# Performance work log

Hardware: AMD Instinct MI355X
Metric: run time of the kernel (lower is better)

Reference implementation:

```python
import jax, jax.numpy as jnp
import numpy as np


def _segment_mean(msg, dst, num_nodes):
    # msg: [E, B, O, T] summed into [N, B, O, T], mean over incoming edges
    s = jax.ops.segment_sum(msg, dst, num_segments=num_nodes)
    cnt = jax.ops.segment_sum(jnp.ones((msg.shape[0],), msg.dtype), dst, num_segments=num_nodes)
    return s / jnp.clip(cnt, 1.0)[:, None, None, None]


def _gcn(x, edge_index, edge_attr, A, Wk, Wr, b):
    # Edge-conditioned (spline-style) graph conv.
    # x: [B, N, Cin, T]; edge_attr: [E, 3]; Wk: [K, Cin, Cout]
    N = x.shape[1]
    src, dst = edge_index[0], edge_index[1]
    Bw = jax.nn.softmax(edge_attr @ A, axis=-1)          # [E, K] basis weights
    We = jnp.einsum('ek,kio->eio', Bw, Wk)                # [E, Cin, Cout]
    msg = jnp.einsum('beit,eio->ebot', x[:, src], We)     # [E, B, Cout, T]
    agg = _segment_mean(msg, dst, N).transpose(1, 0, 2, 3)  # [B, N, Cout, T]
    out = agg + jnp.einsum('bnit,io->bnot', x, Wr) + b[None, None, :, None]
    return jax.nn.elu(out)


def _pool(x, P, C, T):
    # x: [B, N_l, C, T] -> flatten, sparse-pool with P [N_{l+1}, N_l], unflatten
    B, N = x.shape[0], x.shape[1]
    xf = x.reshape(B, N, C * T)
    xf = jnp.einsum('mn,bnf->bmf', P, xf)
    return xf.reshape(B, P.shape[0], C, T)


def setup_inputs() -> dict:
    key = jax.random.key(0)
    ks = jax.random.split(key, 24)
    B, T = 2, 200
    N = [2048, 512, 128, 64]
    E = [16384, 8192, 2048]
    nf = [1, 8, 16, 32, 64, 128, 128]
    ld = 64

    def rn(k, shape, scale=1.0):
        return jax.random.normal(k, shape, dtype=jnp.float32) * scale

    inp = {}
    inp['x'] = rn(ks[0], (B, N[0], nf[0], T))
    inp['ei0'] = jax.random.randint(ks[1], (2, E[0]), 0, N[0])
    inp['ea0'] = jax.random.uniform(ks[2], (E[0], 3), dtype=jnp.float32)
    inp['ei1'] = jax.random.randint(ks[3], (2, E[1]), 0, N[1])
    inp['ea1'] = jax.random.uniform(ks[4], (E[1], 3), dtype=jnp.float32)
    inp['ei2'] = jax.random.randint(ks[5], (2, E[2]), 0, N[2])
    inp['ea2'] = jax.random.uniform(ks[6], (E[2], 3), dtype=jnp.float32)
    # gcn params: (A basis map, K=3 kernel weights, root weight, bias)
    inp['A1'] = rn(ks[7], (3, 3))
    inp['Wk1'] = rn(ks[8], (3, nf[0], nf[2]), 1.0 / np.sqrt(nf[0]))
    inp['Wr1'] = rn(ks[9], (nf[0], nf[2]), 1.0 / np.sqrt(nf[0]))
    inp['b1'] = jnp.zeros((nf[2],), jnp.float32)
    inp['A2'] = rn(ks[10], (3, 3))
    inp['Wk2'] = rn(ks[11], (3, nf[2], nf[3]), 1.0 / np.sqrt(nf[2]))
    inp['Wr2'] = rn(ks[12], (nf[2], nf[3]), 1.0 / np.sqrt(nf[2]))
    inp['b2'] = jnp.zeros((nf[3],), jnp.float32)
    inp['A3'] = rn(ks[13], (3, 3))
    inp['Wk3'] = rn(ks[14], (3, nf[3], nf[4]), 1.0 / np.sqrt(nf[3]))
    inp['Wr3'] = rn(ks[15], (nf[3], nf[4]), 1.0 / np.sqrt(nf[3]))
    inp['b3'] = jnp.zeros((nf[4],), jnp.float32)
    # sparse pooling projections (dense here)
    inp['P01'] = rn(ks[16], (N[1], N[0]), 1.0 / np.sqrt(N[0]))
    inp['P12'] = rn(ks[17], (N[2], N[1]), 1.0 / np.sqrt(N[1]))
    inp['P23'] = rn(ks[18], (N[3], N[2]), 1.0 / np.sqrt(N[2]))
    # 1x1 conv encoder head
    inp['fce1_w'] = rn(ks[19], (nf[4], nf[6]), 1.0 / np.sqrt(nf[4]))
    inp['fce1_b'] = jnp.zeros((nf[6],), jnp.float32)
    inp['fce2_w'] = rn(ks[20], (nf[6], ld), 1.0 / np.sqrt(nf[6]))
    inp['fce2_b'] = jnp.zeros((ld,), jnp.float32)
    return inp


def reference(x, ei0, ea0, ei1, ea1, ei2, ea2, A1, Wk1, Wr1, b1, A2, Wk2, Wr2, b2,
              A3, Wk3, Wr3, b3, P01, P12, P23, fce1_w, fce1_b, fce2_w, fce2_b):
    T = x.shape[-1]
    # level 0 -> 1
    h = _gcn(x, ei0, ea0, A1, Wk1, Wr1, b1)          # [B, N0, 16, T]
    h = _pool(h, P01, h.shape[2], T)                 # [B, N1, 16, T]
    # level 1 -> 2
    h = _gcn(h, ei1, ea1, A2, Wk2, Wr2, b2)          # [B, N1, 32, T]
    h = _pool(h, P12, h.shape[2], T)                 # [B, N2, 32, T]
    # level 2 -> 3
    h = _gcn(h, ei2, ea2, A3, Wk3, Wr3, b3)          # [B, N2, 64, T]
    h = _pool(h, P23, h.shape[2], T)                 # [B, N3, 64, T]
    # 1x1 conv encoder head (channel-wise linear over node/time grid)
    h = jax.nn.elu(jnp.einsum('bnct,co->bnot', h, fce1_w) + fce1_b[None, None, :, None])
    mu = jnp.tanh(jnp.einsum('bnct,co->bnot', h, fce2_w) + fce2_b[None, None, :, None])
    return mu  # [B, N3, latent_dim, T]
```

## Files before the change

### kernel.cpp

```cpp
#include <hip/hip_runtime.h>
#include <hip/hip_bf16.h>

using bf16 = __hip_bfloat16;
typedef unsigned short ushort_t;
typedef unsigned int uint_t;

constexpr int B = 2, T = 200;
constexpr int N0 = 2048, N1 = 512, N2 = 128, N3 = 64;
constexpr int E0 = 16384, E1 = 8192, E2 = 2048;

typedef __attribute__((ext_vector_type(8))) short bf16x8;
typedef __attribute__((ext_vector_type(4))) float f32x4;

constexpr size_t O_FLAG = 161792;
constexpr size_t O_WC1  = 163840;
constexpr size_t O_BIAS = 164096;
constexpr size_t O_BW0  = 165312;
constexpr size_t O_BW1  = 361920;
constexpr size_t O_BW2  = 460224;
constexpr size_t O_PB1  = 484800;
constexpr size_t O_PB2  = 2581952;
constexpr size_t O_PB3  = 2713024;
constexpr size_t O_WT2  = 2729408;
constexpr size_t O_WT3  = 2733504;
constexpr size_t O_W1H  = 2749888;
constexpr size_t O_W2H  = 2766272;
constexpr size_t O_AA   = 2785280;
constexpr size_t O_BB   = 15892480;

__device__ __forceinline__ float ldx(const void* p, long i, int bf) {
  if (bf) {
    uint_t v = (uint_t)(((const ushort_t*)p)[i]) << 16;
    float f; __builtin_memcpy(&f, &v, 4); return f;
  }
  return ((const float*)p)[i];
}
__device__ __forceinline__ ushort_t f2bfu(float v) {
  bf16 h = __float2bfloat16(v); ushort_t u; __builtin_memcpy(&u, &h, 2); return u;
}

struct InPtrs {
  const void* ea0; const void* ea1; const void* ea2;
  const void* P01; const void* P12; const void* P23;
  const void* Wk1; const void* Wr1; const void* Wk2; const void* Wr2;
  const void* Wk3; const void* Wr3; const void* W1h; const void* W2h;
  const void* b1; const void* b2; const void* b3; const void* b1h; const void* b2h;
  const void* A1; const void* A2; const void* A3;
};

__global__ void k_setup0(int* I, const ushort_t* ea) {
  if (blockIdx.x < 158) {
    int i = blockIdx.x * 256 + threadIdx.x;
    I[i] = 0;
  } else if (threadIdx.x == 0) {
    int c = 0;
    for (int i = 0; i < 128; ++i) {
      uint_t v = (uint_t)ea[i] << 16;
      float f; __builtin_memcpy(&f, &v, 4);
      if (f >= 0.f && f <= 1.0f) c++;
    }
    *(int*)((char*)I + O_FLAG) = (c >= 120) ? 1 : 0;
  }
}

__device__ __forceinline__ void bw_one(const void* ea, int bf, const void* A,
                                       float* bw, int e) {
  float a0 = ldx(ea, e*3+0, bf), a1 = ldx(ea, e*3+1, bf), a2 = ldx(ea, e*3+2, bf);
  float l0 = a0*ldx(A,0,bf) + a1*ldx(A,3,bf) + a2*ldx(A,6,bf);
  float l1 = a0*ldx(A,1,bf) + a1*ldx(A,4,bf) + a2*ldx(A,7,bf);
  float l2 = a0*ldx(A,2,bf) + a1*ldx(A,5,bf) + a2*ldx(A,8,bf);
  float m = fmaxf(l0, fmaxf(l1, l2));
  float x0 = expf(l0 - m), x1 = expf(l1 - m), x2 = expf(l2 - m);
  float inv = 1.0f / (x0 + x1 + x2);
  bw[e*3+0] = x0*inv; bw[e*3+1] = x1*inv; bw[e*3+2] = x2*inv;
}

__global__ void k_prep(InPtrs P, char* base) {
  int bf = *(const int*)(base + O_FLAG);
  int bx = blockIdx.x, tid = threadIdx.x;
  float* bw0 = (float*)(base + O_BW0);
  float* bw1 = (float*)(base + O_BW1);
  float* bw2 = (float*)(base + O_BW2);
  if (bx < 64)        { bw_one(P.ea0, bf, P.A1, bw0, bx*256+tid); return; }
  if (bx < 96)        { bw_one(P.ea1, bf, P.A2, bw1, (bx-64)*256+tid); return; }
  if (bx < 104)       { bw_one(P.ea2, bf, P.A3, bw2, (bx-96)*256+tid); return; }
  if (bx < 4200)      { long i = (long)(bx-104)*256+tid;
                        ((ushort_t*)(base+O_PB1))[i] = f2bfu(ldx(P.P01, i, bf)); return; }
  if (bx < 4456)      { int i = (bx-4200)*256+tid;
                        ((ushort_t*)(base+O_PB2))[i] = f2bfu(ldx(P.P12, i, bf)); return; }
  if (bx < 4488)      { int i = (bx-4456)*256+tid;
                        ((ushort_t*)(base+O_PB3))[i] = f2bfu(ldx(P.P23, i, bf)); return; }
  if (bx < 4496)      { int j = (bx-4488)*256+tid; int o = j>>6, c = j&63;
                        float v = (c<48) ? ldx(P.Wk2, c*32+o, bf) : ldx(P.Wr2, (c-48)*32+o, bf);
                        ((ushort_t*)(base+O_WT2))[j] = f2bfu(v); return; }
  if (bx < 4528)      { int j = (bx-4496)*256+tid; int o = j>>7, c = j&127;
                        float v = (c<96) ? ldx(P.Wk3, c*64+o, bf) : ldx(P.Wr3, (c-96)*64+o, bf);
                        ((ushort_t*)(base+O_WT3))[j] = f2bfu(v); return; }
  if (bx < 4560)      { int j = (bx-4528)*256+tid; int o = j>>6, c = j&63;
                        ((ushort_t*)(base+O_W1H))[j] = f2bfu(ldx(P.W1h, c*128+o, bf)); return; }
  if (bx < 4592)      { int j = (bx-4560)*256+tid; int o = j>>7, c = j&127;
                        ((ushort_t*)(base+O_W2H))[j] = f2bfu(ldx(P.W2h, c*64+o, bf)); return; }
  {
    int i = (bx-4592)*256+tid;
    if (i < 64) {
      ((float*)(base+O_WC1))[i] = (i<48) ? ldx(P.Wk1, i, bf) : ldx(P.Wr1, i-48, bf);
    } else if (i < 368) {
      int j = i - 64; float v;
      if (j < 16)       v = ldx(P.b1, j, bf);
      else if (j < 48)  v = ldx(P.b2, j-16, bf);
      else if (j < 112) v = ldx(P.b3, j-48, bf);
      else if (j < 240) v = ldx(P.b1h, j-112, bf);
      else              v = ldx(P.b2h, j-240, bf);
      ((float*)(base+O_BIAS))[j] = v;
    }
  }
}

__global__ void k_hist3(const int* d0, const int* d1, const int* d2,
                        int* c0, int* c1, int* c2) {
  int i = blockIdx.x * 256 + threadIdx.x;
  if (i < E0) atomicAdd(&c0[d0[i]], 1);
  if (i < E1) atomicAdd(&c1[d1[i]], 1);
  if (i < E2) atomicAdd(&c2[d2[i]], 1);
}

__global__ void k_scan3(const int* c0, int* o0, int* u0,
                        const int* c1, int* o1, int* u1,
                        const int* c2, int* o2, int* u2) {
  const int* cnt; int* off; int* cur; int N;
  if (blockIdx.x == 0)      { cnt = c0; off = o0; cur = u0; N = N0; }
  else if (blockIdx.x == 1) { cnt = c1; off = o1; cur = u1; N = N1; }
  else                      { cnt = c2; off = o2; cur = u2; N = N2; }
  int tid = threadIdx.x;
  int chunk = (N + 63) >> 6;
  int base = tid * chunk;
  int s = 0;
  for (int j = 0; j < chunk; ++j) { int idx = base + j; if (idx < N) s += cnt[idx]; }
  int pre = s;
  for (int d = 1; d < 64; d <<= 1) {
    int v = __shfl_up(pre, d, 64);
    if (tid >= d) pre += v;
  }
  int run = pre - s;
  for (int j = 0; j < chunk; ++j) {
    int idx = base + j;
    if (idx < N) { off[idx] = run; cur[idx] = run; run += cnt[idx]; }
  }
  if (tid == 63) off[N] = run;
}

__global__ void k_fill3(const int* d0, int* u0, int* e0l,
                        const int* d1, int* u1, int* e1l,
                        const int* d2, int* u2, int* e2l) {
  int i = blockIdx.x * 256 + threadIdx.x;
  if (i < E0) { int p = atomicAdd(&u0[d0[i]], 1); e0l[p] = i; }
  if (i < E1) { int p = atomicAdd(&u1[d1[i]], 1); e1l[p] = i; }
  if (i < E2) { int p = atomicAdd(&u2[d2[i]], 1); e2l[p] = i; }
}

__global__ __launch_bounds__(256) void k_gc1(const void* x, const int* src,
    const int* off, const int* elist, const int* cnt, const float* bw,
    const float* W, const float* bias, bf16* h1, const int* flagp) {
  __shared__ float Wl[64];
  __shared__ float bl[16];
  __shared__ float ew0[32], ew1[32], ew2[32];
  __shared__ int es[32];
  int tid = threadIdx.x;
  if (tid < 64) Wl[tid] = W[tid];
  if (tid < 16) bl[tid] = bias[tid];
  int bf = *flagp;
  int n = blockIdx.y, b = blockIdx.z;
  int t = tid;
  bool tok = t < T;
  int beg = off[n], end = off[n + 1];
  float a0 = 0.f, a1 = 0.f, a2 = 0.f;
  for (int q0 = beg; q0 < end; q0 += 32) {
    int m = end - q0; if (m > 32) m = 32;
    __syncthreads();
    if (tid < m) {
      int e = elist[q0 + tid];
      es[tid] = src[e];
      ew0[tid] = bw[e*3+0]; ew1[tid] = bw[e*3+1]; ew2[tid] = bw[e*3+2];
    }
    __syncthreads();
    if (tok) {
      for (int j = 0; j < m; ++j) {
        float xv = ldx(x, (long)(b * N0 + es[j]) * T + t, bf);
        a0 += ew0[j] * xv; a1 += ew1[j] * xv; a2 += ew2[j] * xv;
      }
    }
  }
  __syncthreads();
  if (!tok) return;
  int c = cnt[n];
  float inv = 1.f / (float)(c > 0 ? c : 1);
  a0 *= inv; a1 *= inv; a2 *= inv;
  float xr = ldx(x, (long)(b * N0 + n) * T + t, bf);
  bf16* op = h1 + ((long)(b * N0 + n) * 16) * T + t;
#pragma unroll
  for (int o = 0; o < 16; ++o) {
    float v = a0 * Wl[o] + a1 * Wl[16 + o] + a2 * Wl[32 + o] + xr * Wl[48 + o] + bl[o];
    v = v > 0.f ? v : (expf(v) - 1.f);
    op[o * T] = __float2bfloat16(v);
  }
}

template<int CIN, int CPI, int O>
__global__ __launch_bounds__(256) void k_gcm(const float* hp, const int* src,
    const int* off, const int* elist, const int* cnt, const float* bw,
    const ushort_t* Wt, const float* bias, bf16* h, int N) {
  constexpr int C = 4 * CIN;
  constexpr int KG = C / 8;
  constexpr int MT = O / 16;
  __shared__ __align__(16) ushort_t Ws[O * C];
  __shared__ __align__(16) ushort_t Is[64 * C];
  __shared__ float ew0[32], ew1[32], ew2[32];
  __shared__ int es[32];
  int tid = threadIdx.x;
  int w = tid >> 6, l = tid & 63;
  int lf = l & 15, quad = l >> 4;
  int t0 = blockIdx.x * 64;
  int n = blockIdx.y, b = blockIdx.z;
  {
    const uint4* Wg = (const uint4*)Wt;
    for (int s = tid; s < O * KG; s += 256) {
      int o = s / KG, kg = s % KG;
      *(uint4*)(Ws + o * C + ((kg ^ (o & 7)) * 8)) = Wg[s];
    }
  }
  int tx = tid & 63, iy = tid >> 6;
  int t = t0 + tx;
  bool tok = t < T;
  float acc[3][CPI], xr[CPI];
#pragma unroll
  for (int k = 0; k < 3; ++k)
#pragma unroll
    for (int j = 0; j < CPI; ++j) acc[k][j] = 0.f;
#pragma unroll
  for (int j = 0; j < CPI; ++j) xr[j] = 0.f;
  int beg = off[n], end = off[n + 1];
  for (int q0 = beg; q0 < end; q0 += 32) {
    int mE = end - q0; if (mE > 32) mE = 32;
    __syncthreads();
    if (tid < mE) {
      int e = elist[q0 + tid];
      es[tid] = src[e];
      ew0[tid] = bw[e*3+0]; ew1[tid] = bw[e*3+1]; ew2[tid] = bw[e*3+2];
    }
    __syncthreads();
    if (tok) {
      for (int j2 = 0; j2 < mE; ++j2) {
        int s = es[j2];
        float w0 = ew0[j2], w1 = ew1[j2], w2 = ew2[j2];
        const float* xp = hp + ((long)(b * N + s) * CIN) * T + t;
#pragma unroll
        for (int j = 0; j < CPI; ++j) {
          float xv = xp[(iy * CPI + j) * T];
          acc[0][j] += w0 * xv; acc[1][j] += w1 * xv; acc[2][j] += w2 * xv;
        }
      }
    }
  }
  float inv = 1.f;
  if (tok) {
    int c = cnt[n];
    inv = 1.f / (float)(c > 0 ? c : 1);
    const float* xs = hp + ((long)(b * N + n) * CIN) * T + t;
#pragma unroll
    for (int j = 0; j < CPI; ++j) xr[j] = xs[(iy * CPI + j) * T];
  }
#pragma unroll
  for (int j = 0; j < CPI; ++j) {
    int i = iy * CPI + j;
#pragma unroll
    for (int k = 0; k < 3; ++k) {
      int c = k * CIN + i;
      Is[tx * C + ((c >> 3) ^ (tx & 7)) * 8 + (c & 7)] = f2bfu(acc[k][j] * inv);
    }
    int c = 3 * CIN + i;
    Is[tx * C + ((c >> 3) ^ (tx & 7)) * 8 + (c & 7)] = f2bfu(xr[j]);
  }
  __syncthreads();
  f32x4 dacc[MT];
#pragma unroll
  for (int mt = 0; mt < MT; ++mt) dacc[mt] = (f32x4){0.f, 0.f, 0.f, 0.f};
  int tr = w * 16 + lf;
#pragma unroll
  for (int kc = 0; kc < C / 32; ++kc) {
    int kg0 = kc * 4 + quad;
    bf16x8 bfr = *(const bf16x8*)(Is + tr * C + ((kg0 ^ (tr & 7)) * 8));
#pragma unroll
    for (int mt = 0; mt < MT; ++mt) {
      int o = mt * 16 + lf;
      bf16x8 afr = *(const bf16x8*)(Ws + o * C + ((kg0 ^ (o & 7)) * 8));
      dacc[mt] = __builtin_amdgcn_mfma_f32_16x16x32_bf16(afr, bfr, dacc[mt], 0, 0, 0);
    }
  }
  int tg = t0 + w * 16 + lf;
  if (tg < T) {
    long nb = (long)(b * N + n) * O;
#pragma unroll
    for (int mt = 0; mt < MT; ++mt) {
#pragma unroll
      for (int r = 0; r < 4; ++r) {
        int o = mt * 16 + quad * 4 + r;
        float v = dacc[mt][r] + bias[o];
        v = v > 0.f ? v : (expf(v) - 1.f);
        h[(nb + o) * T + tg] = __float2bfloat16(v);
      }
    }
  }
}

template<int FT>
__global__ __launch_bounds__(256) void k_poolw(const ushort_t* __restrict__ Pb,
    const ushort_t* __restrict__ h, float* __restrict__ out,
    int M, int K, int F, int nInner) {
  constexpr int BN = 16 * FT;
  constexpr int NOCT = BN / 8;
  constexpr int NROW = 256 / NOCT;
  constexpr int NP = 64 / NROW;
  __shared__ __align__(16) ushort_t As[64 * 64];
  __shared__ __align__(16) ushort_t Bs[BN * 64];
  int tid = threadIdx.x;
  int w = tid >> 6, l = tid & 63;
  int lf = l & 15, quad = l >> 4;
  int ml = w * 16 + lf;
  int v = blockIdx.x;
  { int q = gridDim.x >> 3; v = (v & 7) * q + (v >> 3); }
  int f_blk = v / nInner; int rem = v - f_blk * nInner;
  int m_blk = rem >> 1;
  int b = rem & 1;
  int f0 = f_blk * BN, m0 = m_blk * 64;

  int am0 = tid >> 3, ak = tid & 7;
  int am1 = am0 + 32;
  const ushort_t* Ap0 = Pb + (long)(m0 + am0) * K + ak * 8;
  const ushort_t* Ap1 = Pb + (long)(m0 + am1) * K + ak * 8;
  int wofA0 = am0 * 64 + ((ak ^ (am0 & 7)) * 8);
  int wofA1 = am1 * 64 + ((ak ^ (am1 & 7)) * 8);
  int fo = tid % NOCT;
  int krb = tid / NOCT;
  const ushort_t* Bp = h + ((long)b * K + krb) * F + f0 + fo * 8;

  f32x4 acc[FT];
#pragma unroll
  for (int ft = 0; ft < FT; ++ft) acc[ft] = (f32x4){0.f, 0.f, 0.f, 0.f};

  for (int kk = 0; kk < K; kk += 64) {
    uint4 a0 = *(const uint4*)(Ap0 + kk);
    uint4 a1 = *(const uint4*)(Ap1 + kk);
    uint4 bv[NP];
#pragma unroll
    for (int p = 0; p < NP; ++p)
      bv[p] = *(const uint4*)(Bp + (long)(kk + p * NROW) * F);
    __syncthreads();
    *(uint4*)(As + wofA0) = a0;
    *(uint4*)(As + wofA1) = a1;
#pragma unroll
    for (int p = 0; p < NP; ++p) {
      int kr = krb + p * NROW;
      int kh = kr >> 3, kw = kr & 7;
#pragma unroll
      for (int j = 0; j < 8; ++j) {
        int f = fo * 8 + j;
        int sw = j ^ fo;
        Bs[f * 64 + ((kh ^ sw) * 8) + kw] = ((const ushort_t*)&bv[p])[j];
      }
    }
    __syncthreads();
#pragma unroll
    for (int ks = 0; ks < 2; ++ks) {
      int kq = ks * 4 + quad;
      bf16x8 bfr[FT];
#pragma unroll
      for (int ft = 0; ft < FT; ++ft) {
        int fl = ft * 16 + lf;
        int sfl = (fl & 7) ^ ((fl >> 3) & 7);
        bfr[ft] = *(const bf16x8*)(Bs + fl * 64 + ((kq ^ sfl) * 8));
      }
      bf16x8 afr = *(const bf16x8*)(As + ml * 64 + ((kq ^ (ml & 7)) * 8));
#pragma unroll
      for (int ft = 0; ft < FT; ++ft)
        acc[ft] = __builtin_amdgcn_mfma_f32_16x16x32_bf16(afr, bfr[ft], acc[ft], 0, 0, 0);
    }
  }

#pragma unroll
  for (int rr = 0; rr < 4; ++rr) {
    int m = m0 + w * 16 + quad * 4 + rr;
    float* op = out + ((long)(b * M + m)) * F + f0 + lf;
#pragma unroll
    for (int ft = 0; ft < FT; ++ft) op[ft * 16] = acc[ft][rr];
  }
}

__global__ __launch_bounds__(256) void k_head(const float* hp3, const ushort_t* W1t,
    const ushort_t* W2t, const float* bias, void* outp, const int* flagp) {
  __shared__ __align__(16) ushort_t Ws1[128 * 64];
  __shared__ __align__(16) ushort_t Ws2[64 * 128];
  __shared__ __align__(16) ushort_t Is[64 * 64];
  __shared__ __align__(16) ushort_t G[64 * 128];
  int tid = threadIdx.x;
  int w = tid >> 6, l = tid & 63;
  int lf = l & 15, quad = l >> 4;
  int t0 = blockIdx.x * 64;
  int n = blockIdx.y, b = blockIdx.z;
  {
    const uint4* g1 = (const uint4*)W1t;
    for (int s = tid; s < 1024; s += 256) {
      int o = s >> 3, kg = s & 7;
      *(uint4*)(Ws1 + o * 64 + ((kg ^ (o & 7)) * 8)) = g1[s];
    }
    const uint4* g2 = (const uint4*)W2t;
    for (int s = tid; s < 1024; s += 256) {
      int o = s >> 4, kg = s & 15;
      *(uint4*)(Ws2 + o * 128 + ((kg ^ (o & 7)) * 8)) = g2[s];
    }
  }
  {
    int t = tid & 63;
    bool tok = (t0 + t) < T;
    const float* ip = hp3 + ((long)(b * 64 + n) * 64) * T + t0;
    for (int kg = tid >> 6; kg < 8; kg += 4) {
      ushort_t r[8];
#pragma unroll
      for (int j = 0; j < 8; ++j)
        r[j] = tok ? f2bfu(ip[(kg * 8 + j) * T + t]) : (ushort_t)0;
      *(uint4*)(Is + t * 64 + ((kg ^ (t & 7)) * 8)) = *(uint4*)r;
    }
  }
  __syncthreads();
  int tr = w * 16 + lf;
  {
    f32x4 a1[8];
#pragma unroll
    for (int mt = 0; mt < 8; ++mt) a1[mt] = (f32x4){0.f, 0.f, 0.f, 0.f};
#pragma unroll
    for (int kc = 0; kc < 2; ++kc) {
      int kg0 = kc * 4 + quad;
      bf16x8 bfr = *(const bf16x8*)(Is + tr * 64 + ((kg0 ^ (tr & 7)) * 8));
#pragma unroll
      for (int mt = 0; mt < 8; ++mt) {
        int o = mt * 16 + lf;
        bf16x8 afr = *(const bf16x8*)(Ws1 + o * 64 + ((kg0 ^ (o & 7)) * 8));
        a1[mt] = __builtin_amdgcn_mfma_f32_16x16x32_bf16(afr, bfr, a1[mt], 0, 0, 0);
      }
    }
    int tG = w * 16 + lf;
#pragma unroll
    for (int mt = 0; mt < 8; ++mt) {
#pragma unroll
      for (int r = 0; r < 4; ++r) {
        int o1 = mt * 16 + quad * 4 + r;
        float v = a1[mt][r] + bias[112 + o1];
        v = v > 0.f ? v : (expf(v) - 1.f);
        G[tG * 128 + ((o1 >> 3) ^ (tG & 7)) * 8 + (o1 & 7)] = f2bfu(v);
      }
    }
  }
  __syncthreads();
  {
    f32x4 a2[4];
#pragma unroll
    for (int mt = 0; mt < 4; ++mt) a2[mt] = (f32x4){0.f, 0.f, 0.f, 0.f};
#pragma unroll
    for (int kc = 0; kc < 4; ++kc) {
      int kg0 = kc * 4 + quad;
      bf16x8 bfr = *(const bf16x8*)(G + tr * 128 + ((kg0 ^ (tr & 7)) * 8));
#pragma unroll
      for (int mt = 0; mt < 4; ++mt) {
        int o = mt * 16 + lf;
        bf16x8 afr = *(const bf16x8*)(Ws2 + o * 128 + ((kg0 ^ (o & 7)) * 8));
        a2[mt] = __builtin_amdgcn_mfma_f32_16x16x32_bf16(afr, bfr, a2[mt], 0, 0, 0);
      }
    }
    int t = t0 + w * 16 + lf;
    if (t < T) {
      int bf = *flagp;
      long nb = (long)(b * 64 + n) * 64;
#pragma unroll
      for (int mt = 0; mt < 4; ++mt) {
#pragma unroll
        for (int r = 0; r < 4; ++r) {
          int o2 = mt * 16 + quad * 4 + r;
          float v = tanhf(a2[mt][r] + bias[240 + o2]);
          long idx = (nb + o2) * T + t;
          if (bf) ((bf16*)outp)[idx] = __float2bfloat16(v);
          else    ((float*)outp)[idx] = v;
        }
      }
    }
  }
}

extern "C" void kernel_launch(void* const* d_in, const int* in_sizes, int n_in,
                              void* d_out, int out_size, void* d_ws, size_t ws_size,
                              hipStream_t stream) {
  const int* ei0 = (const int*)d_in[1];
  const int* ei1 = (const int*)d_in[3];
  const int* ei2 = (const int*)d_in[5];

  char* base = (char*)d_ws;
  int* I = (int*)base;
  int* cnt0 = I;         int* off0 = I + 2048;  int* cur0 = I + 4112;  int* el0 = I + 6160;
  int* cnt1 = I + 22544; int* off1 = I + 23056; int* cur1 = I + 23584; int* el1 = I + 24096;
  int* cnt2 = I + 32288; int* off2 = I + 32416; int* cur2 = I + 32560; int* el2 = I + 32688;
  const int* flagp = (const int*)(base + O_FLAG);
  float* wc1f = (float*)(base + O_WC1);
  float* bias = (float*)(base + O_BIAS);
  float* bw0 = (float*)(base + O_BW0);
  float* bw1 = (float*)(base + O_BW1);
  float* bw2 = (float*)(base + O_BW2);
  ushort_t* Pb1 = (ushort_t*)(base + O_PB1);
  ushort_t* Pb2 = (ushort_t*)(base + O_PB2);
  ushort_t* Pb3 = (ushort_t*)(base + O_PB3);
  ushort_t* wt2 = (ushort_t*)(base + O_WT2);
  ushort_t* wt3 = (ushort_t*)(base + O_WT3);
  ushort_t* w1t = (ushort_t*)(base + O_W1H);
  ushort_t* w2t = (ushort_t*)(base + O_W2H);
  char* Aa = base + O_AA;
  char* Bb = base + O_BB;

  InPtrs P = { d_in[2], d_in[4], d_in[6], d_in[19], d_in[20], d_in[21],
               d_in[8], d_in[9], d_in[12], d_in[13], d_in[16], d_in[17],
               d_in[22], d_in[24], d_in[10], d_in[14], d_in[18], d_in[23],
               d_in[25], d_in[7], d_in[11], d_in[15] };

  k_setup0<<<159, 256, 0, stream>>>(I, (const ushort_t*)d_in[2]);
  k_prep<<<4594, 256, 0, stream>>>(P, base);
  k_hist3<<<64, 256, 0, stream>>>(ei0 + E0, ei1 + E1, ei2 + E2, cnt0, cnt1, cnt2);
  k_scan3<<<3, 64, 0, stream>>>(cnt0, off0, cur0, cnt1, off1, cur1, cnt2, off2, cur2);
  k_fill3<<<64, 256, 0, stream>>>(ei0 + E0, cur0, el0, ei1 + E1, cur1, el1, ei2 + E2, cur2, el2);

  k_gc1<<<dim3(1, N0, B), 256, 0, stream>>>(d_in[0], ei0, off0, el0, cnt0, bw0, wc1f, bias, (bf16*)Bb, flagp);
  k_poolw<2><<<1600, 256, 0, stream>>>(Pb1, (const ushort_t*)Bb, (float*)Aa, 512, 2048, 3200, 16);
  k_gcm<16, 4, 32><<<dim3(4, N1, B), 256, 0, stream>>>((const float*)Aa, ei1, off1, el1, cnt1, bw1, wt2, bias + 16, (bf16*)Bb, N1);
  k_poolw<2><<<800, 256, 0, stream>>>(Pb2, (const ushort_t*)Bb, (float*)Aa, 128, 512, 6400, 4);
  k_gcm<32, 8, 64><<<dim3(4, N2, B), 256, 0, stream>>>((const float*)Aa, ei2, off2, el2, cnt2, bw2, wt3, bias + 48, (bf16*)Bb, N2);
  k_poolw<2><<<800, 256, 0, stream>>>(Pb3, (const ushort_t*)Bb, (float*)Aa, 64, 128, 12800, 2);
  k_head<<<dim3(4, N3, B), 256, 0, stream>>>((const float*)Aa, w1t, w2t, bias, d_out, flagp);
}
```

Before: 286.8 us.

## Restructure pooling GEMM with larger tiles, double-buffered B and direct A loads

Replaces the pooling GEMM kernel with one that uses 64-wide feature tiles and up to 128-row M tiles per block. The B operand (activations) is double-buffered in LDS with register prefetch, so there is one barrier per K step. The A operand (pool matrix) is read straight from global memory into MFMA fragments instead of being staged in LDS. This cuts block count and redundant B loads and overlaps global loads with MFMA work. The costs are fewer blocks per grid, which lowers occupancy and parallelism, and uncoalesced 2-byte strided global loads for B.

```diff
diff --git a/kernel.cpp b/kernel.cpp
--- a/kernel.cpp
+++ b/kernel.cpp
@@ -312,86 +312,87 @@
   }
 }
 
-template<int FT>
-__global__ __launch_bounds__(256) void k_poolw(const ushort_t* __restrict__ Pb,
+template<int WMT>
+__global__ __launch_bounds__(256) void k_poolx(const ushort_t* __restrict__ Pb,
     const ushort_t* __restrict__ h, float* __restrict__ out,
     int M, int K, int F, int nInner) {
-  constexpr int BN = 16 * FT;
-  constexpr int NOCT = BN / 8;
-  constexpr int NROW = 256 / NOCT;
-  constexpr int NP = 64 / NROW;
-  __shared__ __align__(16) ushort_t As[64 * 64];
-  __shared__ __align__(16) ushort_t Bs[BN * 64];
+  __shared__ __align__(16) ushort_t Bs0[64 * 64];
+  __shared__ __align__(16) ushort_t Bs1[64 * 64];
   int tid = threadIdx.x;
   int w = tid >> 6, l = tid & 63;
   int lf = l & 15, quad = l >> 4;
-  int ml = w * 16 + lf;
   int v = blockIdx.x;
   { int q = gridDim.x >> 3; v = (v & 7) * q + (v >> 3); }
   int f_blk = v / nInner; int rem = v - f_blk * nInner;
   int m_blk = rem >> 1;
   int b = rem & 1;
-  int f0 = f_blk * BN, m0 = m_blk * 64;
-
-  int am0 = tid >> 3, ak = tid & 7;
-  int am1 = am0 + 32;
-  const ushort_t* Ap0 = Pb + (long)(m0 + am0) * K + ak * 8;
-  const ushort_t* Ap1 = Pb + (long)(m0 + am1) * K + ak * 8;
-  int wofA0 = am0 * 64 + ((ak ^ (am0 & 7)) * 8);
-  int wofA1 = am1 * 64 + ((ak ^ (am1 & 7)) * 8);
-  int fo = tid % NOCT;
-  int krb = tid / NOCT;
-  const ushort_t* Bp = h + ((long)b * K + krb) * F + f0 + fo * 8;
-
-  f32x4 acc[FT];
-#pragma unroll
-  for (int ft = 0; ft < FT; ++ft) acc[ft] = (f32x4){0.f, 0.f, 0.f, 0.f};
-
-  for (int kk = 0; kk < K; kk += 64) {
-    uint4 a0 = *(const uint4*)(Ap0 + kk);
-    uint4 a1 = *(const uint4*)(Ap1 + kk);
-    uint4 bv[NP];
-#pragma unroll
-    for (int p = 0; p < NP; ++p)
-      bv[p] = *(const uint4*)(Bp + (long)(kk + p * NROW) * F);
-    __syncthreads();
-    *(uint4*)(As + wofA0) = a0;
-    *(uint4*)(As + wofA1) = a1;
-#pragma unroll
-    for (int p = 0; p < NP; ++p) {
-      int kr = krb + p * NROW;
-      int kh = kr >> 3, kw = kr & 7;
-#pragma unroll
-      for (int j = 0; j < 8; ++j) {
-        int f = fo * 8 + j;
-        int sw = j ^ fo;
-        Bs[f * 64 + ((kh ^ sw) * 8) + kw] = ((const ushort_t*)&bv[p])[j];
-      }
-    }
-    __syncthreads();
+  int f0 = f_blk * 64, m0 = m_blk * (64 * WMT);
+  int nsteps = K >> 6;
+
+  int fB = tid & 63, kb = (tid >> 6) * 16;
+  const ushort_t* Bp = h + ((long)b * K + kb) * F + f0 + fB;
+  int kc0 = kb >> 3;
+  int wofB0 = fB * 64 + ((kc0 ^ (fB & 7)) * 8);
+  int wofB1 = fB * 64 + (((kc0 + 1) ^ (fB & 7)) * 8);
+
+  const ushort_t* Ap[WMT];
+#pragma unroll
+  for (int wm = 0; wm < WMT; ++wm)
+    Ap[wm] = Pb + (long)(m0 + wm * 64 + w * 16 + lf) * K + quad * 8;
+
+  f32x4 acc[WMT][4];
+#pragma unroll
+  for (int wm = 0; wm < WMT; ++wm)
+#pragma unroll
+    for (int ft = 0; ft < 4; ++ft) acc[wm][ft] = (f32x4){0.f, 0.f, 0.f, 0.f};
+
+  ushort_t rb[16];
+#pragma unroll
+  for (int i = 0; i < 16; ++i) rb[i] = Bp[(long)i * F];
+  *(uint4*)(Bs0 + wofB0) = *(uint4*)&rb[0];
+  *(uint4*)(Bs0 + wofB1) = *(uint4*)&rb[8];
+  __syncthreads();
+
+  for (int s = 0; s < nsteps; ++s) {
+    const ushort_t* Bsc = (s & 1) ? Bs1 : Bs0;
+    ushort_t* Bsn = (s & 1) ? Bs0 : Bs1;
+    if (s + 1 < nsteps) {
+#pragma unroll
+      for (int i = 0; i < 16; ++i) rb[i] = Bp[((long)(s + 1) * 64 + i) * F];
+    }
 #pragma unroll
     for (int ks = 0; ks < 2; ++ks) {
       int kq = ks * 4 + quad;
-      bf16x8 bfr[FT];
-#pragma unroll
-      for (int ft = 0; ft < FT; ++ft) {
+      bf16x8 bfr[4];
+#pragma unroll
+      for (int ft = 0; ft < 4; ++ft) {
         int fl = ft * 16 + lf;
-        int sfl = (fl & 7) ^ ((fl >> 3) & 7);
-        bfr[ft] = *(const bf16x8*)(Bs + fl * 64 + ((kq ^ sfl) * 8));
-      }
-      bf16x8 afr = *(const bf16x8*)(As + ml * 64 + ((kq ^ (ml & 7)) * 8));
-#pragma unroll
-      for (int ft = 0; ft < FT; ++ft)
-        acc[ft] = __builtin_amdgcn_mfma_f32_16x16x32_bf16(afr, bfr[ft], acc[ft], 0, 0, 0);
-    }
-  }
-
-#pragma unroll
-  for (int rr = 0; rr < 4; ++rr) {
-    int m = m0 + w * 16 + quad * 4 + rr;
-    float* op = out + ((long)(b * M + m)) * F + f0 + lf;
-#pragma unroll
-    for (int ft = 0; ft < FT; ++ft) op[ft * 16] = acc[ft][rr];
+        bfr[ft] = *(const bf16x8*)(Bsc + fl * 64 + ((kq ^ (fl & 7)) * 8));
+      }
+#pragma unroll
+      for (int wm = 0; wm < WMT; ++wm) {
+        bf16x8 afr = *(const bf16x8*)(Ap[wm] + (long)s * 64 + ks * 32);
+#pragma unroll
+        for (int ft = 0; ft < 4; ++ft)
+          acc[wm][ft] = __builtin_amdgcn_mfma_f32_16x16x32_bf16(afr, bfr[ft], acc[wm][ft], 0, 0, 0);
+      }
+    }
+    if (s + 1 < nsteps) {
+      *(uint4*)(Bsn + wofB0) = *(uint4*)&rb[0];
+      *(uint4*)(Bsn + wofB1) = *(uint4*)&rb[8];
+    }
+    __syncthreads();
+  }
+
+#pragma unroll
+  for (int wm = 0; wm < WMT; ++wm) {
+#pragma unroll
+    for (int rr = 0; rr < 4; ++rr) {
+      int m = m0 + wm * 64 + w * 16 + quad * 4 + rr;
+      float* op = out + ((long)(b * M + m)) * F + f0 + lf;
+#pragma unroll
+      for (int ft = 0; ft < 4; ++ft) op[ft * 16] = acc[wm][ft][rr];
+    }
   }
 }
 
@@ -534,10 +535,10 @@
   k_fill3<<<64, 256, 0, stream>>>(ei0 + E0, cur0, el0, ei1 + E1, cur1, el1, ei2 + E2, cur2, el2);
 
   k_gc1<<<dim3(1, N0, B), 256, 0, stream>>>(d_in[0], ei0, off0, el0, cnt0, bw0, wc1f, bias, (bf16*)Bb, flagp);
-  k_poolw<2><<<1600, 256, 0, stream>>>(Pb1, (const ushort_t*)Bb, (float*)Aa, 512, 2048, 3200, 16);
+  k_poolx<2><<<400, 256, 0, stream>>>(Pb1, (const ushort_t*)Bb, (float*)Aa, 512, 2048, 3200, 8);
   k_gcm<16, 4, 32><<<dim3(4, N1, B), 256, 0, stream>>>((const float*)Aa, ei1, off1, el1, cnt1, bw1, wt2, bias + 16, (bf16*)Bb, N1);
-  k_poolw<2><<<800, 256, 0, stream>>>(Pb2, (const ushort_t*)Bb, (float*)Aa, 128, 512, 6400, 4);
+  k_poolx<2><<<200, 256, 0, stream>>>(Pb2, (const ushort_t*)Bb, (float*)Aa, 128, 512, 6400, 2);
   k_gcm<32, 8, 64><<<dim3(4, N2, B), 256, 0, stream>>>((const float*)Aa, ei2, off2, el2, cnt2, bw2, wt3, bias + 48, (bf16*)Bb, N2);
-  k_poolw<2><<<800, 256, 0, stream>>>(Pb3, (const ushort_t*)Bb, (float*)Aa, 64, 128, 12800, 2);
+  k_poolx<1><<<400, 256, 0, stream>>>(Pb3, (const ushort_t*)Bb, (float*)Aa, 64, 128, 12800, 2);
   k_head<<<dim3(4, N3, B), 256, 0, stream>>>((const float*)Aa, w1t, w2t, bias, d_out, flagp);
 }
```

Result: no change. 291.9 us (+1.8%).
